# Performance work log

Hardware: AMD Instinct MI355X
Metric: run time of the kernel (lower is better)

## Reference

```python
import jax, jax.numpy as jnp
import numpy as np

N_NODES = 100000
N_EDGES = 1600000
IN_DIM, HID, OUT = 6, 64, 32


def _linear_params(key, fan_in, fan_out):
    k1, k2 = jax.random.split(key)
    bound = 1.0 / np.sqrt(fan_in)
    W = jax.random.uniform(k1, (fan_in, fan_out), jnp.float32, -bound, bound)
    b = jax.random.uniform(k2, (fan_out,), jnp.float32, -bound, bound)
    return W, b


def setup_inputs() -> dict:
    key = jax.random.key(0)
    ks = jax.random.split(key, 9)
    x = jax.random.normal(ks[0], (N_NODES, IN_DIM), jnp.float32)
    edge_index = jax.random.randint(ks[1], (2, N_EDGES), 0, N_NODES, jnp.int64)
    edge_attr = jax.random.normal(ks[2], (N_EDGES, 3), jnp.float32)
    W1a, b1a = _linear_params(ks[3], IN_DIM + 3, HID)
    W1b, b1b = _linear_params(ks[4], HID, HID)
    W2a, b2a = _linear_params(ks[5], HID + 3, HID)
    W2b, b2b = _linear_params(ks[6], HID, HID)
    W3a, b3a = _linear_params(ks[7], HID + 3, OUT)
    W3b, b3b = _linear_params(ks[8], OUT, OUT)
    return {
        "x": x, "edge_index": edge_index, "edge_attr": edge_attr,
        "W1a": W1a, "b1a": b1a, "W1b": W1b, "b1b": b1b,
        "W2a": W2a, "b2a": b2a, "W2b": W2b, "b2b": b2b,
        "W3a": W3a, "b3a": b3a, "W3b": W3b, "b3b": b3b,
    }


def _gnn_layer(x, src, dst, edge_attr, Wa, ba, Wb, bb):
    # message: per-edge 2-layer MLP on [x_j, edge_attr]
    msg = jnp.concatenate([x[src], edge_attr], axis=-1)       # [E, in+3]
    h = jax.nn.relu(msg @ Wa + ba) @ Wb + bb                   # [E, out]
    # aggr='mean': scatter-sum into target nodes, divide by in-degree
    s = jax.ops.segment_sum(h, dst, num_segments=N_NODES)     # [N, out]
    cnt = jax.ops.segment_sum(jnp.ones((src.shape[0],), x.dtype), dst,
                              num_segments=N_NODES)
    return s / jnp.maximum(cnt, 1.0)[:, None]


def reference(x, edge_index, edge_attr,
              W1a, b1a, W1b, b1b,
              W2a, b2a, W2b, b2b,
              W3a, b3a, W3b, b3b):
    src, dst = edge_index[0], edge_index[1]   # x_j = x[src], aggregate at dst
    h = _gnn_layer(x, src, dst, edge_attr, W1a, b1a, W1b, b1b)
    h = jax.nn.relu(h)
    h = _gnn_layer(h, src, dst, edge_attr, W2a, b2a, W2b, b2b)
    h = jax.nn.relu(h)
    out = _gnn_layer(h, src, dst, edge_attr, W3a, b3a, W3b, b3b)
    return out
```

## Files before the change

kernel.cpp:

```cpp
#include <hip/hip_runtime.h>
#include <hip/hip_fp16.h>

#define N_NODES 100000
#define N_EDGES 1600000

__global__ __launch_bounds__(256) void degree_kernel(const int* __restrict__ dst,
                                                     int* __restrict__ cnt, int E) {
    int i = blockIdx.x * blockDim.x + threadIdx.x;
    int stride = gridDim.x * blockDim.x;
    for (; i < E; i += stride) atomicAdd(&cnt[dst[i]], 1);
}

__global__ __launch_bounds__(256) void inv_kernel(const int* __restrict__ cnt,
                                                  float* __restrict__ inv, int N) {
    int i = blockIdx.x * blockDim.x + threadIdx.x;
    if (i < N) inv[i] = (cnt[i] > 0) ? (1.0f / (float)cnt[i]) : 0.0f;
}

__global__ __launch_bounds__(256) void block_sum_kernel(const int* __restrict__ cnt,
                                                        int* __restrict__ bsum, int N) {
    __shared__ int s[256];
    const int tid = threadIdx.x;
    const int i = blockIdx.x * 256 + tid;
    s[tid] = (i < N) ? cnt[i] : 0;
    __syncthreads();
#pragma unroll
    for (int d = 128; d > 0; d >>= 1) {
        if (tid < d) s[tid] += s[tid + d];
        __syncthreads();
    }
    if (tid == 0) bsum[blockIdx.x] = s[0];
}

__global__ __launch_bounds__(512) void scan_bsum_kernel(int* __restrict__ bsum, int NB) {
    __shared__ int s[512];
    const int tid = threadIdx.x;
    const int v = (tid < NB) ? bsum[tid] : 0;
    s[tid] = v;
    __syncthreads();
    for (int d = 1; d < 512; d <<= 1) {
        const int t = (tid >= d) ? s[tid - d] : 0;
        __syncthreads();
        s[tid] += t;
        __syncthreads();
    }
    if (tid < NB) bsum[tid] = s[tid] - v;
}

__global__ __launch_bounds__(256) void make_cursor_kernel(const int* __restrict__ cnt,
                                                          const int* __restrict__ bsum,
                                                          int* __restrict__ cursor, int N) {
    __shared__ int s[256];
    const int tid = threadIdx.x;
    const int i = blockIdx.x * 256 + tid;
    const int v = (i < N) ? cnt[i] : 0;
    s[tid] = v;
    __syncthreads();
    for (int d = 1; d < 256; d <<= 1) {
        const int t = (tid >= d) ? s[tid - d] : 0;
        __syncthreads();
        s[tid] += t;
        __syncthreads();
    }
    if (i < N) cursor[i] = bsum[blockIdx.x] + s[tid] - v;
}

__global__ __launch_bounds__(256) void scatter_pack_kernel(
    const int* __restrict__ src, const int* __restrict__ dst,
    const float* __restrict__ ea,
    int* __restrict__ cursor, float4* __restrict__ spf, int E) {
    const int range = blockIdx.x & 7;
    const int lo = range * (N_NODES / 8);
    const int hi = lo + (N_NODES / 8);
    int i = (blockIdx.x >> 3) * blockDim.x + threadIdx.x;
    const int stride = (gridDim.x >> 3) * blockDim.x;
    for (; i < E; i += stride) {
        const int d = dst[i];
        if (d >= lo && d < hi) {
            const int pos = atomicAdd(&cursor[d], 1);
            spf[pos] = make_float4(__int_as_float(src[i]),
                                   ea[3 * (size_t)i + 0],
                                   ea[3 * (size_t)i + 1],
                                   ea[3 * (size_t)i + 2]);
        }
    }
}

__global__ __launch_bounds__(256) void node_gemm6h(
    const float* __restrict__ x, const float* __restrict__ W,
    const float* __restrict__ bias, __half* __restrict__ out_, int N) {
    int n = blockIdx.x * blockDim.x + threadIdx.x;
    if (n >= N) return;
    const float* row = x + (size_t)n * 6;
    float v[6];
#pragma unroll
    for (int k = 0; k < 6; ++k) v[k] = row[k];
    __half2* orow = (__half2*)(out_ + (size_t)n * 64);
    for (int g = 0; g < 16; ++g) {
        float a0 = bias[4 * g + 0], a1 = bias[4 * g + 1];
        float a2 = bias[4 * g + 2], a3 = bias[4 * g + 3];
#pragma unroll
        for (int k = 0; k < 6; ++k) {
            const float m = v[k];
            const float* w = &W[k * 64 + 4 * g];
            a0 = fmaf(m, w[0], a0);
            a1 = fmaf(m, w[1], a1);
            a2 = fmaf(m, w[2], a2);
            a3 = fmaf(m, w[3], a3);
        }
        orow[2 * g]     = __floats2half2_rn(a0, a1);
        orow[2 * g + 1] = __floats2half2_rn(a2, a3);
    }
}

template <int DIN, int DNEXT, bool LAST, bool INH, bool OUTH>
__global__ __launch_bounds__(256) void fused_agg(
    const void* __restrict__ Pv,
    const float4* __restrict__ spf,
    const int* __restrict__ cursor, const int* __restrict__ cnt,
    const float* __restrict__ inv,
    const float* __restrict__ We,
    const float* __restrict__ Wb,
    const float* __restrict__ bb,
    const float* __restrict__ Wn,
    const float* __restrict__ bn,
    void* __restrict__ Poutv, int N) {
    constexpr int NPW = 64 / DIN;
    const float*  Pf = (const float*)Pv;
    const __half* Ph = (const __half*)Pv;
    const int lane = threadIdx.x & 63;
    const int w    = threadIdx.x >> 6;
    const int c    = lane % DIN;
    const int sub  = lane / DIN;
    const int n    = (blockIdx.x * 4 + w) * NPW + sub;

    __shared__ __align__(16) float lrow[4][64];

    const float we0 = We[c], we1 = We[DIN + c], we2 = We[2 * DIN + c];
    const int end   = cursor[n];
    const int count = cnt[n];
    int j = end - count;
    const float s_inv = inv[n];
    const float mask  = (s_inv != 0.0f) ? 1.0f : 0.0f;

    float sum = 0.0f;
    for (; j + 4 <= end; j += 4) {
        const float4 f0 = spf[j];
        const float4 f1 = spf[j + 1];
        const float4 f2 = spf[j + 2];
        const float4 f3 = spf[j + 3];
        const size_t i0 = (size_t)__float_as_int(f0.x) * DIN + c;
        const size_t i1 = (size_t)__float_as_int(f1.x) * DIN + c;
        const size_t i2 = (size_t)__float_as_int(f2.x) * DIN + c;
        const size_t i3 = (size_t)__float_as_int(f3.x) * DIN + c;
        const float p0 = INH ? __half2float(Ph[i0]) : Pf[i0];
        const float p1 = INH ? __half2float(Ph[i1]) : Pf[i1];
        const float p2 = INH ? __half2float(Ph[i2]) : Pf[i2];
        const float p3 = INH ? __half2float(Ph[i3]) : Pf[i3];
        const float h0 = fmaf(f0.w, we2, fmaf(f0.z, we1, fmaf(f0.y, we0, p0)));
        const float h1 = fmaf(f1.w, we2, fmaf(f1.z, we1, fmaf(f1.y, we0, p1)));
        const float h2 = fmaf(f2.w, we2, fmaf(f2.z, we1, fmaf(f2.y, we0, p2)));
        const float h3 = fmaf(f3.w, we2, fmaf(f3.z, we1, fmaf(f3.y, we0, p3)));
        sum += fmaxf(h0, 0.0f) + fmaxf(h1, 0.0f);
        sum += fmaxf(h2, 0.0f) + fmaxf(h3, 0.0f);
    }
    for (; j < end; ++j) {
        const float4 f0 = spf[j];
        const size_t i0 = (size_t)__float_as_int(f0.x) * DIN + c;
        const float p0 = INH ? __half2float(Ph[i0]) : Pf[i0];
        sum += fmaxf(fmaf(f0.w, we2, fmaf(f0.z, we1, fmaf(f0.y, we0, p0))), 0.0f);
    }

    const float t = sum * s_inv;
    lrow[w][lane] = t;
    __builtin_amdgcn_wave_barrier();
    float m = bb[c] * mask;
#pragma unroll
    for (int q = 0; q < DIN / 4; ++q) {
        const float4 r = *(const float4*)&lrow[w][sub * DIN + 4 * q];
        m = fmaf(r.x, Wb[(4 * q + 0) * DIN + c], m);
        m = fmaf(r.y, Wb[(4 * q + 1) * DIN + c], m);
        m = fmaf(r.z, Wb[(4 * q + 2) * DIN + c], m);
        m = fmaf(r.w, Wb[(4 * q + 3) * DIN + c], m);
    }
    if constexpr (LAST) {
        ((float*)Poutv)[(size_t)n * DIN + c] = m;
    } else {
        m = fmaxf(m, 0.0f);
        __builtin_amdgcn_wave_barrier();
        lrow[w][lane] = m;
        __builtin_amdgcn_wave_barrier();
        const int c2 = lane % DNEXT;
        float o = bn[c2];
#pragma unroll
        for (int q = 0; q < DIN / 4; ++q) {
            const float4 r = *(const float4*)&lrow[w][4 * q];
            o = fmaf(r.x, Wn[(4 * q + 0) * DNEXT + c2], o);
            o = fmaf(r.y, Wn[(4 * q + 1) * DNEXT + c2], o);
            o = fmaf(r.z, Wn[(4 * q + 2) * DNEXT + c2], o);
            o = fmaf(r.w, Wn[(4 * q + 3) * DNEXT + c2], o);
        }
        if (lane < DNEXT) {
            if constexpr (OUTH)
                ((__half*)Poutv)[(size_t)n * DNEXT + lane] = __float2half_rn(o);
            else
                ((float*)Poutv)[(size_t)n * DNEXT + lane] = o;
        }
    }
}

extern "C" void kernel_launch(void* const* d_in, const int* in_sizes, int n_in,
                              void* d_out, int out_size, void* d_ws, size_t ws_size,
                              hipStream_t stream) {
    const float* x   = (const float*)d_in[0];
    const int*   ei  = (const int*)d_in[1];
    const float* ea  = (const float*)d_in[2];
    const float* W1a = (const float*)d_in[3];
    const float* b1a = (const float*)d_in[4];
    const float* W1b = (const float*)d_in[5];
    const float* b1b = (const float*)d_in[6];
    const float* W2a = (const float*)d_in[7];
    const float* b2a = (const float*)d_in[8];
    const float* W2b = (const float*)d_in[9];
    const float* b2b = (const float*)d_in[10];
    const float* W3a = (const float*)d_in[11];
    const float* b3a = (const float*)d_in[12];
    const float* W3b = (const float*)d_in[13];
    const float* b3b = (const float*)d_in[14];

    const int* src = ei;
    const int* dst = ei + N_EDGES;
    float* out = (float*)d_out;

    char* ws = (char*)d_ws;
    int*    cnt    = (int*)(ws);
    float*  inv    = (float*)(ws + 0x80000);
    int*    bsum   = (int*)(ws + 0x100000);
    int*    cursor = (int*)(ws + 0x110000);
    float4* spf    = (float4*)(ws + 0x200000);
    __half* PH1    = (__half*)(ws + 0x1B00000);
    __half* PH2    = (__half*)(ws + 0x2800000);
    float*  P3     = (float*)(ws + 0x3500000);

    const int NBLK = (N_NODES + 255) / 256;

    hipMemsetAsync(cnt, 0, N_NODES * sizeof(int), stream);
    degree_kernel<<<2048, 256, 0, stream>>>(dst, cnt, N_EDGES);
    inv_kernel<<<NBLK, 256, 0, stream>>>(cnt, inv, N_NODES);
    block_sum_kernel<<<NBLK, 256, 0, stream>>>(cnt, bsum, N_NODES);
    scan_bsum_kernel<<<1, 512, 0, stream>>>(bsum, NBLK);
    make_cursor_kernel<<<NBLK, 256, 0, stream>>>(cnt, bsum, cursor, N_NODES);
    scatter_pack_kernel<<<2048, 256, 0, stream>>>(src, dst, ea, cursor, spf, N_EDGES);

    node_gemm6h<<<NBLK, 256, 0, stream>>>(x, W1a, b1a, PH1, N_NODES);

    fused_agg<64, 64, false, true, true><<<N_NODES / 4, 256, 0, stream>>>(
        PH1, spf, cursor, cnt, inv, W1a + 6 * 64, W1b, b1b, W2a, b2a, PH2, N_NODES);
    fused_agg<64, 32, false, true, false><<<N_NODES / 4, 256, 0, stream>>>(
        PH2, spf, cursor, cnt, inv, W2a + 64 * 64, W2b, b2b, W3a, b3a, P3, N_NODES);
    fused_agg<32, 32, true, false, false><<<N_NODES / 8, 256, 0, stream>>>(
        P3, spf, cursor, cnt, inv, W3a + 64 * 32, W3b, b3b, nullptr, nullptr, out, N_NODES);
}
```

Measured before the change: 519.3 us.

## Split edge gather across lane quarters with vectorized feature loads and shuffle reduce

Restructures the aggregation kernels so each wave processes one node with four edges in flight at once. Each lane loads a 4-wide half vector (or a 2-wide float vector) of the source feature row instead of a single scalar, and the four partial sums are combined with xor shuffles. This cuts the number of serial edge iterations per wave and the per-element gather instruction count, which targets gather latency. In exchange it adds shuffle reductions and more registers for the edge weights, and the last layer now uses one node per wave instead of two.

```diff
diff --git a/kernel.cpp b/kernel.cpp
--- a/kernel.cpp
+++ b/kernel.cpp
@@ -113,9 +113,9 @@
     }
 }
 
-template <int DIN, int DNEXT, bool LAST, bool INH, bool OUTH>
-__global__ __launch_bounds__(256) void fused_agg(
-    const void* __restrict__ Pv,
+template <int DNEXT, bool OUTH>
+__global__ __launch_bounds__(256) void fused_agg64(
+    const __half* __restrict__ P,
     const float4* __restrict__ spf,
     const int* __restrict__ cursor, const int* __restrict__ cnt,
     const float* __restrict__ inv,
@@ -125,88 +125,160 @@
     const float* __restrict__ Wn,
     const float* __restrict__ bn,
     void* __restrict__ Poutv, int N) {
-    constexpr int NPW = 64 / DIN;
-    const float*  Pf = (const float*)Pv;
-    const __half* Ph = (const __half*)Pv;
     const int lane = threadIdx.x & 63;
     const int w    = threadIdx.x >> 6;
-    const int c    = lane % DIN;
-    const int sub  = lane / DIN;
-    const int n    = (blockIdx.x * 4 + w) * NPW + sub;
+    const int q    = lane >> 4;
+    const int p    = lane & 15;
+    const int n    = blockIdx.x * 4 + w;
 
     __shared__ __align__(16) float lrow[4][64];
 
-    const float we0 = We[c], we1 = We[DIN + c], we2 = We[2 * DIN + c];
+    float we0[4], we1[4], we2[4];
+#pragma unroll
+    for (int k = 0; k < 4; ++k) {
+        we0[k] = We[0 * 64 + 4 * p + k];
+        we1[k] = We[1 * 64 + 4 * p + k];
+        we2[k] = We[2 * 64 + 4 * p + k];
+    }
+
     const int end   = cursor[n];
     const int count = cnt[n];
     int j = end - count;
     const float s_inv = inv[n];
     const float mask  = (s_inv != 0.0f) ? 1.0f : 0.0f;
 
-    float sum = 0.0f;
-    for (; j + 4 <= end; j += 4) {
-        const float4 f0 = spf[j];
-        const float4 f1 = spf[j + 1];
-        const float4 f2 = spf[j + 2];
-        const float4 f3 = spf[j + 3];
-        const size_t i0 = (size_t)__float_as_int(f0.x) * DIN + c;
-        const size_t i1 = (size_t)__float_as_int(f1.x) * DIN + c;
-        const size_t i2 = (size_t)__float_as_int(f2.x) * DIN + c;
-        const size_t i3 = (size_t)__float_as_int(f3.x) * DIN + c;
-        const float p0 = INH ? __half2float(Ph[i0]) : Pf[i0];
-        const float p1 = INH ? __half2float(Ph[i1]) : Pf[i1];
-        const float p2 = INH ? __half2float(Ph[i2]) : Pf[i2];
-        const float p3 = INH ? __half2float(Ph[i3]) : Pf[i3];
-        const float h0 = fmaf(f0.w, we2, fmaf(f0.z, we1, fmaf(f0.y, we0, p0)));
-        const float h1 = fmaf(f1.w, we2, fmaf(f1.z, we1, fmaf(f1.y, we0, p1)));
-        const float h2 = fmaf(f2.w, we2, fmaf(f2.z, we1, fmaf(f2.y, we0, p2)));
-        const float h3 = fmaf(f3.w, we2, fmaf(f3.z, we1, fmaf(f3.y, we0, p3)));
-        sum += fmaxf(h0, 0.0f) + fmaxf(h1, 0.0f);
-        sum += fmaxf(h2, 0.0f) + fmaxf(h3, 0.0f);
-    }
-    for (; j < end; ++j) {
-        const float4 f0 = spf[j];
-        const size_t i0 = (size_t)__float_as_int(f0.x) * DIN + c;
-        const float p0 = INH ? __half2float(Ph[i0]) : Pf[i0];
-        sum += fmaxf(fmaf(f0.w, we2, fmaf(f0.z, we1, fmaf(f0.y, we0, p0))), 0.0f);
-    }
-
-    const float t = sum * s_inv;
-    lrow[w][lane] = t;
+    float s0 = 0.f, s1 = 0.f, s2 = 0.f, s3 = 0.f;
+
+#define GRP4H(base)                                                              \
+    {                                                                            \
+        const float4 f = spf[(base) + q];                                        \
+        const ushort4 raw = *(const ushort4*)((const unsigned short*)P +         \
+                            ((size_t)__float_as_int(f.x) << 6) + 4 * p);         \
+        const float p0 = __half2float(__ushort_as_half(raw.x));                  \
+        const float p1 = __half2float(__ushort_as_half(raw.y));                  \
+        const float p2 = __half2float(__ushort_as_half(raw.z));                  \
+        const float p3 = __half2float(__ushort_as_half(raw.w));                  \
+        s0 += fmaxf(fmaf(f.w, we2[0], fmaf(f.z, we1[0], fmaf(f.y, we0[0], p0))), 0.f); \
+        s1 += fmaxf(fmaf(f.w, we2[1], fmaf(f.z, we1[1], fmaf(f.y, we0[1], p1))), 0.f); \
+        s2 += fmaxf(fmaf(f.w, we2[2], fmaf(f.z, we1[2], fmaf(f.y, we0[2], p2))), 0.f); \
+        s3 += fmaxf(fmaf(f.w, we2[3], fmaf(f.z, we1[3], fmaf(f.y, we0[3], p3))), 0.f); \
+    }
+
+    for (; j + 8 <= end; j += 8) { GRP4H(j) GRP4H(j + 4) }
+    if (j + 4 <= end) { GRP4H(j) j += 4; }
+    const int rem = end - j;
+    if (q < rem) { GRP4H(j) }
+#undef GRP4H
+
+    s0 += __shfl_xor(s0, 16); s1 += __shfl_xor(s1, 16);
+    s2 += __shfl_xor(s2, 16); s3 += __shfl_xor(s3, 16);
+    s0 += __shfl_xor(s0, 32); s1 += __shfl_xor(s1, 32);
+    s2 += __shfl_xor(s2, 32); s3 += __shfl_xor(s3, 32);
+
+    if (lane < 16) {
+        *(float4*)&lrow[w][4 * p] =
+            make_float4(s0 * s_inv, s1 * s_inv, s2 * s_inv, s3 * s_inv);
+    }
     __builtin_amdgcn_wave_barrier();
+
+    float m = bb[lane] * mask;
+#pragma unroll
+    for (int k = 0; k < 16; ++k) {
+        const float4 r = *(const float4*)&lrow[w][4 * k];
+        m = fmaf(r.x, Wb[(4 * k + 0) * 64 + lane], m);
+        m = fmaf(r.y, Wb[(4 * k + 1) * 64 + lane], m);
+        m = fmaf(r.z, Wb[(4 * k + 2) * 64 + lane], m);
+        m = fmaf(r.w, Wb[(4 * k + 3) * 64 + lane], m);
+    }
+    m = fmaxf(m, 0.0f);
+    __builtin_amdgcn_wave_barrier();
+    lrow[w][lane] = m;
+    __builtin_amdgcn_wave_barrier();
+    const int c2 = lane % DNEXT;
+    float o = bn[c2];
+#pragma unroll
+    for (int k = 0; k < 16; ++k) {
+        const float4 r = *(const float4*)&lrow[w][4 * k];
+        o = fmaf(r.x, Wn[(4 * k + 0) * DNEXT + c2], o);
+        o = fmaf(r.y, Wn[(4 * k + 1) * DNEXT + c2], o);
+        o = fmaf(r.z, Wn[(4 * k + 2) * DNEXT + c2], o);
+        o = fmaf(r.w, Wn[(4 * k + 3) * DNEXT + c2], o);
+    }
+    if (lane < DNEXT) {
+        if constexpr (OUTH)
+            ((__half*)Poutv)[(size_t)n * DNEXT + lane] = __float2half_rn(o);
+        else
+            ((float*)Poutv)[(size_t)n * DNEXT + lane] = o;
+    }
+}
+
+__global__ __launch_bounds__(256) void fused_agg32(
+    const float* __restrict__ P,
+    const float4* __restrict__ spf,
+    const int* __restrict__ cursor, const int* __restrict__ cnt,
+    const float* __restrict__ inv,
+    const float* __restrict__ We,
+    const float* __restrict__ Wb,
+    const float* __restrict__ bb,
+    float* __restrict__ out, int N) {
+    const int lane = threadIdx.x & 63;
+    const int w    = threadIdx.x >> 6;
+    const int q    = lane >> 4;
+    const int p    = lane & 15;
+    const int n    = blockIdx.x * 4 + w;
+
+    __shared__ __align__(16) float lrow[4][32];
+
+    float we0[2], we1[2], we2[2];
+#pragma unroll
+    for (int k = 0; k < 2; ++k) {
+        we0[k] = We[0 * 32 + 2 * p + k];
+        we1[k] = We[1 * 32 + 2 * p + k];
+        we2[k] = We[2 * 32 + 2 * p + k];
+    }
+
+    const int end   = cursor[n];
+    const int count = cnt[n];
+    int j = end - count;
+    const float s_inv = inv[n];
+    const float mask  = (s_inv != 0.0f) ? 1.0f : 0.0f;
+
+    float s0 = 0.f, s1 = 0.f;
+
+#define GRP4F(base)                                                              \
+    {                                                                            \
+        const float4 f = spf[(base) + q];                                        \
+        const float2 pr = *(const float2*)(P +                                   \
+                          ((size_t)__float_as_int(f.x) << 5) + 2 * p);           \
+        s0 += fmaxf(fmaf(f.w, we2[0], fmaf(f.z, we1[0], fmaf(f.y, we0[0], pr.x))), 0.f); \
+        s1 += fmaxf(fmaf(f.w, we2[1], fmaf(f.z, we1[1], fmaf(f.y, we0[1], pr.y))), 0.f); \
+    }
+
+    for (; j + 8 <= end; j += 8) { GRP4F(j) GRP4F(j + 4) }
+    if (j + 4 <= end) { GRP4F(j) j += 4; }
+    const int rem = end - j;
+    if (q < rem) { GRP4F(j) }
+#undef GRP4F
+
+    s0 += __shfl_xor(s0, 16); s1 += __shfl_xor(s1, 16);
+    s0 += __shfl_xor(s0, 32); s1 += __shfl_xor(s1, 32);
+
+    if (lane < 16) {
+        *(float2*)&lrow[w][2 * p] = make_float2(s0 * s_inv, s1 * s_inv);
+    }
+    __builtin_amdgcn_wave_barrier();
+
+    const int c = lane & 31;
     float m = bb[c] * mask;
 #pragma unroll
-    for (int q = 0; q < DIN / 4; ++q) {
-        const float4 r = *(const float4*)&lrow[w][sub * DIN + 4 * q];
-        m = fmaf(r.x, Wb[(4 * q + 0) * DIN + c], m);
-        m = fmaf(r.y, Wb[(4 * q + 1) * DIN + c], m);
-        m = fmaf(r.z, Wb[(4 * q + 2) * DIN + c], m);
-        m = fmaf(r.w, Wb[(4 * q + 3) * DIN + c], m);
-    }
-    if constexpr (LAST) {
-        ((float*)Poutv)[(size_t)n * DIN + c] = m;
-    } else {
-        m = fmaxf(m, 0.0f);
-        __builtin_amdgcn_wave_barrier();
-        lrow[w][lane] = m;
-        __builtin_amdgcn_wave_barrier();
-        const int c2 = lane % DNEXT;
-        float o = bn[c2];
-#pragma unroll
-        for (int q = 0; q < DIN / 4; ++q) {
-            const float4 r = *(const float4*)&lrow[w][4 * q];
-            o = fmaf(r.x, Wn[(4 * q + 0) * DNEXT + c2], o);
-            o = fmaf(r.y, Wn[(4 * q + 1) * DNEXT + c2], o);
-            o = fmaf(r.z, Wn[(4 * q + 2) * DNEXT + c2], o);
-            o = fmaf(r.w, Wn[(4 * q + 3) * DNEXT + c2], o);
-        }
-        if (lane < DNEXT) {
-            if constexpr (OUTH)
-                ((__half*)Poutv)[(size_t)n * DNEXT + lane] = __float2half_rn(o);
-            else
-                ((float*)Poutv)[(size_t)n * DNEXT + lane] = o;
-        }
-    }
+    for (int k = 0; k < 8; ++k) {
+        const float4 r = *(const float4*)&lrow[w][4 * k];
+        m = fmaf(r.x, Wb[(4 * k + 0) * 32 + c], m);
+        m = fmaf(r.y, Wb[(4 * k + 1) * 32 + c], m);
+        m = fmaf(r.z, Wb[(4 * k + 2) * 32 + c], m);
+        m = fmaf(r.w, Wb[(4 * k + 3) * 32 + c], m);
+    }
+    if (lane < 32) out[(size_t)n * 32 + c] = m;
 }
 
 extern "C" void kernel_launch(void* const* d_in, const int* in_sizes, int n_in,
@@ -254,10 +326,10 @@
 
     node_gemm6h<<<NBLK, 256, 0, stream>>>(x, W1a, b1a, PH1, N_NODES);
 
-    fused_agg<64, 64, false, true, true><<<N_NODES / 4, 256, 0, stream>>>(
+    fused_agg64<64, true><<<N_NODES / 4, 256, 0, stream>>>(
         PH1, spf, cursor, cnt, inv, W1a + 6 * 64, W1b, b1b, W2a, b2a, PH2, N_NODES);
-    fused_agg<64, 32, false, true, false><<<N_NODES / 4, 256, 0, stream>>>(
+    fused_agg64<32, false><<<N_NODES / 4, 256, 0, stream>>>(
         PH2, spf, cursor, cnt, inv, W2a + 64 * 64, W2b, b2b, W3a, b3a, P3, N_NODES);
-    fused_agg<32, 32, true, false, false><<<N_NODES / 8, 256, 0, stream>>>(
-        P3, spf, cursor, cnt, inv, W3a + 64 * 32, W3b, b3b, nullptr, nullptr, out, N_NODES);
-}
+    fused_agg32<<<N_NODES / 4, 256, 0, stream>>>(
+        P3, spf, cursor, cnt, inv, W3a + 64 * 32, W3b, b3b, out, N_NODES);
+}
```

Measured after the change: 490.1 us. 5.6% less time.
